# Performance work log

Hardware: AMD Instinct MI355X
Metric: run time of the kernel (lower is better)

The kernel has to match this reference:

```python
import jax, jax.numpy as jnp
import numpy as np

U, DP, TOPK, NH = 2, 16, 8, 2
D = 512
M = DP ** U          # 256 slots
DK = U * DP          # 32 addressing dim
BETA_MAX = 2.0


def setup_inputs():
    key = jax.random.key(0)
    ks = jax.random.split(key, 12)
    B, T = 8, 128
    s = 0.02
    return {
        "h": jax.random.normal(ks[0], (B, T, D), jnp.float32),
        "K_slots": jax.random.normal(ks[1], (B, M, D), jnp.float32) * s,
        "V_slots": jax.random.normal(ks[2], (B, M, D), jnp.float32) * s,
        "z_K": jnp.ones((B, M), jnp.float32),
        "z_V": jnp.ones((B, M), jnp.float32),
        "W_k": jax.random.normal(ks[3], (DK, D), jnp.float32) * s,
        "W_q": jax.random.normal(ks[4], (DK, D), jnp.float32) * s,
        "log_tau_w": jnp.zeros((1,), jnp.float32),
        "log_tau_r": jnp.zeros((1,), jnp.float32),
        "hh_k": jax.random.normal(ks[5], (NH, D, D), jnp.float32) * s,
        "hh_vk": jax.random.normal(ks[6], (NH, D, D), jnp.float32) * s,
        "hh_vv": jax.random.normal(ks[7], (NH, D, D), jnp.float32) * s,
        "hh_bw": jax.random.normal(ks[8], (NH, 1, D), jnp.float32) * s,
        "hh_bb": jnp.zeros((NH, 1), jnp.float32),
        "gamma": jnp.float32(1.0),
        "W_out": jax.random.normal(ks[9], (D, D), jnp.float32) * s,
        "W_gate": jax.random.normal(ks[10], (D, D), jnp.float32) * s,
    }


def _kron_address(z, log_tau):
    # z: [B, DK]; Kronecker-factored softmax address over M = DP**U slots
    B = z.shape[0]
    probs = jax.nn.softmax(z.reshape(B, U, DP) / jnp.exp(log_tau[0]), axis=-1)
    addr = probs[:, 0]
    for u in range(1, U):
        addr = (addr[:, :, None] * probs[:, u, None, :]).reshape(B, -1)
    w, idx = jax.lax.top_k(addr, TOPK)
    return idx, w


def _forward(h, K_slots, V_slots, z_K, z_V, W_k, W_q, log_tau_w, log_tau_r,
             hh_k, hh_vk, hh_vv, hh_bw, hh_bb, gamma, W_out, W_gate,
             checkpoint=False):
    B, T, _ = h.shape
    scale = D ** -0.5
    b_idx = jnp.arange(B)[:, None]
    sp_gamma = jax.nn.softplus(gamma)

    def step(carry, h_t):
        K_s, V_s, zK, zV = carry
        write_idx, write_w = _kron_address(h_t @ W_k.T, log_tau_w)
        read_idx, _ = _kron_address(h_t @ W_q.T, log_tau_r)
        # scatter write weights into dense [B, M] (top-k indices are unique)
        w_full = jnp.zeros((B, M), h_t.dtype).at[b_idx, write_idx].set(write_w)
        # PDMA decay
        decay = (1.0 - w_full) ** sp_gamma
        K_s = decay[..., None] * K_s
        V_s = decay[..., None] * V_s
        zK = decay * zK + w_full
        zV = decay * zV + w_full
        # gather active slots: [B, K, D]
        K_act = jnp.take_along_axis(K_s, write_idx[:, :, None], axis=1)
        V_act = jnp.take_along_axis(V_s, write_idx[:, :, None], axis=1)
        # Householder update chain
        for j in range(NH):
            k_j = jax.nn.silu(h_t @ hh_k[j].T)
            k_hat = k_j / jnp.maximum(
                jnp.linalg.norm(k_j, axis=-1, keepdims=True), 1e-12)
            v_kj = h_t @ hh_vk[j].T
            v_vj = h_t @ hh_vv[j].T
            beta = BETA_MAX * jax.nn.sigmoid(h_t @ hh_bw[j].T + hh_bb[j])  # [B,1]
            kh = k_hat[:, None, :]
            be = beta[:, None, :]
            K_act = K_act - be * kh * (kh * K_act).sum(-1, keepdims=True) \
                    + be * k_j[:, None, :] * v_kj[:, None, :]
            V_act = V_act - be * kh * (kh * V_act).sum(-1, keepdims=True) \
                    + be * k_j[:, None, :] * v_vj[:, None, :]
        # scatter updated slots back
        K_s = K_s.at[b_idx, write_idx].set(K_act)
        V_s = V_s.at[b_idx, write_idx].set(V_act)
        # read path
        K_read = jnp.take_along_axis(K_s, read_idx[:, :, None], axis=1)
        V_read = jnp.take_along_axis(V_s, read_idx[:, :, None], axis=1)
        zK_read = jnp.take_along_axis(zK, read_idx, axis=1)[..., None]
        zV_read = jnp.take_along_axis(zV, read_idx, axis=1)[..., None]
        K_n = K_read / zK_read
        V_n = V_read / zV_read
        rel = (K_n * h_t[:, None, :]).sum(-1)           # [B, K]
        attn = jax.nn.softmax(rel * scale, axis=-1)
        readout = (attn[..., None] * V_n).sum(1)        # [B, D]
        out = jax.nn.sigmoid(h_t @ W_gate.T) * (readout @ W_out.T)
        return (K_s, V_s, zK, zV), (out, write_idx, read_idx)

    step_fn = jax.checkpoint(step) if checkpoint else step
    (K_s, V_s, zK, zV), (outs, widx, ridx) = jax.lax.scan(
        step_fn, (K_slots, V_slots, z_K, z_V), jnp.swapaxes(h, 0, 1))
    return (jnp.swapaxes(outs, 0, 1), K_s, V_s, zK, zV, widx[-1], ridx[-1])


def reference(h, K_slots, V_slots, z_K, z_V, W_k, W_q, log_tau_w, log_tau_r,
              hh_k, hh_vk, hh_vv, hh_bw, hh_bb, gamma, W_out, W_gate):
    return _forward(h, K_slots, V_slots, z_K, z_V, W_k, W_q, log_tau_w,
                    log_tau_r, hh_k, hh_vk, hh_vv, hh_bw, hh_bb, gamma,
                    W_out, W_gate)
```

## Files before the change

kernel.cpp:

```cpp
#include <hip/hip_runtime.h>
#include <math.h>

#define D_ 512
#define M_ 256
#define T_ 128
#define B_ 8
#define TOPK_ 8
#define NH_ 2
#define BT_ (B_*T_)

__device__ __forceinline__ float wred(float v){
#pragma unroll
  for (int m = 1; m < 64; m <<= 1) v += __shfl_xor(v, m, 64);
  return v;
}
__device__ __forceinline__ float4 ld4(const float* p){ return *(const float4*)p; }
__device__ __forceinline__ void st4(float* p, float4 v){ *(float4*)p = v; }
__device__ __forceinline__ float dot4(float4 a, float4 b){
  return a.x*b.x + a.y*b.y + a.z*b.z + a.w*b.w;
}
__device__ __forceinline__ float4 scl4(float4 a, float s){
  a.x*=s; a.y*=s; a.z*=s; a.w*=s; return a;
}

template<int CTRL>
__device__ __forceinline__ float dpp_add(float x){
  int y = __builtin_amdgcn_update_dpp(0, __float_as_int(x), CTRL, 0xf, 0xf, true);
  return x + __int_as_float(y);
}
__device__ __forceinline__ float wredd(float x){
  x = dpp_add<0x111>(x);
  x = dpp_add<0x112>(x);
  x = dpp_add<0x114>(x);
  x = dpp_add<0x118>(x);
  x = dpp_add<0x142>(x);
  x = dpp_add<0x143>(x);
  return __int_as_float(__builtin_amdgcn_readlane(__float_as_int(x), 63));
}

__global__ __launch_bounds__(64) void addr_kernel(
    const float* __restrict__ h, const float* __restrict__ Wk,
    const float* __restrict__ Wq, const float* __restrict__ ltw,
    const float* __restrict__ ltr, const float* __restrict__ gammap,
    float* __restrict__ metab)
{
  const int bt = blockIdx.x;
  const int tid = threadIdx.x;
  __shared__ float p_s[64];

  const float* hrow = h + (size_t)bt*D_;
  const float* wrow = (tid < 32) ? (Wk + (size_t)tid*D_)
                                 : (Wq + (size_t)(tid-32)*D_);
  float dot = 0.f;
  for (int d = 0; d < D_; d += 4){
    float4 hv = ld4(&hrow[d]); float4 wv = ld4(&wrow[d]);
    dot += hv.x*wv.x + hv.y*wv.y + hv.z*wv.z + hv.w*wv.w;
  }
  float tau = (tid < 32) ? expf(ltw[0]) : expf(ltr[0]);
  float mx = dot;
#pragma unroll
  for (int m = 1; m < 16; m <<= 1) mx = fmaxf(mx, __shfl_xor(mx, m, 64));
  float e = expf((dot - mx)/tau);
  float sm = e;
#pragma unroll
  for (int m = 1; m < 16; m <<= 1) sm += __shfl_xor(sm, m, 64);
  p_s[tid] = e / sm;
  __syncthreads();

  const int half = tid >> 5;
  const int l = tid & 31;
  const int g0 = half*32, g1 = half*32 + 16;
  float av[8];
#pragma unroll
  for (int k = 0; k < 8; ++k){
    int x = l*8 + k;
    av[k] = p_s[g0 + (x>>4)] * p_s[g1 + (x&15)];
  }
  const float sp = log1pf(expf(gammap[0]));
  for (int r = 0; r < TOPK_; ++r){
    float bv = -1.f; int bi = 0;
#pragma unroll
    for (int k = 0; k < 8; ++k){ if (av[k] > bv){ bv = av[k]; bi = l*8+k; } }
#pragma unroll
    for (int m = 1; m < 32; m <<= 1){
      float ov = __shfl_xor(bv, m, 64); int oi = __shfl_xor(bi, m, 64);
      if (ov > bv || (ov == bv && oi < bi)){ bv = ov; bi = oi; }
    }
    if ((bi >> 3) == l) av[bi & 7] = -2.f;
    float* mp = metab + (size_t)(bt*TOPK_ + r)*4;
    if (tid == 0){
      mp[0] = __int_as_float(bi); mp[1] = bv; mp[2] = powf(1.f - bv, sp);
    }
    if (tid == 32) mp[3] = __int_as_float(bi);
  }
}

__global__ __launch_bounds__(256) void zscan_kernel(
    const float* __restrict__ zK0, const float* __restrict__ zV0,
    const float* __restrict__ metab, float2* __restrict__ zr,
    float* __restrict__ o_zK, float* __restrict__ o_zV)
{
  __shared__ __align__(16) float4 meta_s[T_*TOPK_];
  const int b = blockIdx.x;
  const int m = threadIdx.x;
  const float4* mb = (const float4*)metab + (size_t)b*T_*TOPK_;
#pragma unroll
  for (int q = 0; q < 4; ++q) meta_s[m + q*256] = mb[m + q*256];
  float zk = zK0[b*M_+m], zv = zV0[b*M_+m];
  __syncthreads();
  for (int t = 0; t < T_; ++t){
#pragma unroll
    for (int i = 0; i < TOPK_; ++i){
      float4 me = meta_s[t*TOPK_+i];
      if (m == __float_as_int(me.x)){ zk = me.z*zk + me.y; zv = me.z*zv + me.y; }
    }
#pragma unroll
    for (int i = 0; i < TOPK_; ++i){
      float4 me = meta_s[t*TOPK_+i];
      if (m == __float_as_int(me.w))
        zr[(size_t)(b*T_+t)*TOPK_+i] = make_float2(1.f/zk, 1.f/zv);
    }
  }
  o_zK[b*M_+m] = zk; o_zV[b*M_+m] = zv;
}

struct GemmPtrs { const float* W[6]; float* C[6]; };

__global__ __launch_bounds__(256) void gemm_nt(
    const float* __restrict__ A, GemmPtrs p)
{
  const float* W = p.W[blockIdx.z];
  float* C = p.C[blockIdx.z];
  const int n0 = blockIdx.x * 64;
  const int m0 = blockIdx.y * 64;
  const int tid = threadIdx.x;
  __shared__ __align__(16) float As[16][68];
  __shared__ __align__(16) float Bs[16][68];
  const int r  = tid >> 2;
  const int c4 = (tid & 3) << 2;
  const int tx4 = (tid & 15) << 2;
  const int ty4 = (tid >> 4) << 2;
  float acc[4][4] = {{0.f}};

  for (int kc = 0; kc < 512; kc += 16){
    float4 av = ld4(&A[(size_t)(m0+r)*512 + kc + c4]);
    float4 wv = ld4(&W[(size_t)(n0+r)*512 + kc + c4]);
    __syncthreads();
    As[c4+0][r]=av.x; As[c4+1][r]=av.y; As[c4+2][r]=av.z; As[c4+3][r]=av.w;
    Bs[c4+0][r]=wv.x; Bs[c4+1][r]=wv.y; Bs[c4+2][r]=wv.z; Bs[c4+3][r]=wv.w;
    __syncthreads();
#pragma unroll
    for (int k = 0; k < 16; ++k){
      float4 a  = ld4(&As[k][ty4]);
      float4 bq = ld4(&Bs[k][tx4]);
      acc[0][0]+=a.x*bq.x; acc[0][1]+=a.x*bq.y; acc[0][2]+=a.x*bq.z; acc[0][3]+=a.x*bq.w;
      acc[1][0]+=a.y*bq.x; acc[1][1]+=a.y*bq.y; acc[1][2]+=a.y*bq.z; acc[1][3]+=a.y*bq.w;
      acc[2][0]+=a.z*bq.x; acc[2][1]+=a.z*bq.y; acc[2][2]+=a.z*bq.z; acc[2][3]+=a.z*bq.w;
      acc[3][0]+=a.w*bq.x; acc[3][1]+=a.w*bq.y; acc[3][2]+=a.w*bq.z; acc[3][3]+=a.w*bq.w;
    }
  }
#pragma unroll
  for (int i = 0; i < 4; ++i){
    float4 cv; cv.x=acc[i][0]; cv.y=acc[i][1]; cv.z=acc[i][2]; cv.w=acc[i][3];
    st4(&C[(size_t)(m0+ty4+i)*512 + n0 + tx4], cv);
  }
}

__global__ __launch_bounds__(256) void gemm_out(
    const float* __restrict__ h, const float* __restrict__ rdo,
    const float* __restrict__ Wg, const float* __restrict__ Wo,
    float* __restrict__ C)
{
  const int n0 = blockIdx.x * 64;
  const int m0 = blockIdx.y * 64;
  const int tid = threadIdx.x;
  __shared__ __align__(16) float Ag[16][68];
  __shared__ __align__(16) float Ao[16][68];
  __shared__ __align__(16) float Bg[16][68];
  __shared__ __align__(16) float Bo[16][68];
  const int r  = tid >> 2;
  const int c4 = (tid & 3) << 2;
  const int tx4 = (tid & 15) << 2;
  const int ty4 = (tid >> 4) << 2;
  float accg[4][4] = {{0.f}};
  float acco[4][4] = {{0.f}};

  for (int kc = 0; kc < 512; kc += 16){
    float4 a1 = ld4(&h  [(size_t)(m0+r)*512 + kc + c4]);
    float4 a2 = ld4(&rdo[(size_t)(m0+r)*512 + kc + c4]);
    float4 w1 = ld4(&Wg [(size_t)(n0+r)*512 + kc + c4]);
    float4 w2 = ld4(&Wo [(size_t)(n0+r)*512 + kc + c4]);
    __syncthreads();
    Ag[c4+0][r]=a1.x; Ag[c4+1][r]=a1.y; Ag[c4+2][r]=a1.z; Ag[c4+3][r]=a1.w;
    Ao[c4+0][r]=a2.x; Ao[c4+1][r]=a2.y; Ao[c4+2][r]=a2.z; Ao[c4+3][r]=a2.w;
    Bg[c4+0][r]=w1.x; Bg[c4+1][r]=w1.y; Bg[c4+2][r]=w1.z; Bg[c4+3][r]=w1.w;
    Bo[c4+0][r]=w2.x; Bo[c4+1][r]=w2.y; Bo[c4+2][r]=w2.z; Bo[c4+3][r]=w2.w;
    __syncthreads();
#pragma unroll
    for (int k = 0; k < 16; ++k){
      float4 ag = ld4(&Ag[k][ty4]);
      float4 ao = ld4(&Ao[k][ty4]);
      float4 bg = ld4(&Bg[k][tx4]);
      float4 bo = ld4(&Bo[k][tx4]);
      accg[0][0]+=ag.x*bg.x; accg[0][1]+=ag.x*bg.y; accg[0][2]+=ag.x*bg.z; accg[0][3]+=ag.x*bg.w;
      accg[1][0]+=ag.y*bg.x; accg[1][1]+=ag.y*bg.y; accg[1][2]+=ag.y*bg.z; accg[1][3]+=ag.y*bg.w;
      accg[2][0]+=ag.z*bg.x; accg[2][1]+=ag.z*bg.y; accg[2][2]+=ag.z*bg.z; accg[2][3]+=ag.z*bg.w;
      accg[3][0]+=ag.w*bg.x; accg[3][1]+=ag.w*bg.y; accg[3][2]+=ag.w*bg.z; accg[3][3]+=ag.w*bg.w;
      acco[0][0]+=ao.x*bo.x; acco[0][1]+=ao.x*bo.y; acco[0][2]+=ao.x*bo.z; acco[0][3]+=ao.x*bo.w;
      acco[1][0]+=ao.y*bo.x; acco[1][1]+=ao.y*bo.y; acco[1][2]+=ao.y*bo.z; acco[1][3]+=ao.y*bo.w;
      acco[2][0]+=ao.z*bo.x; acco[2][1]+=ao.z*bo.y; acco[2][2]+=ao.z*bo.z; acco[2][3]+=ao.z*bo.w;
      acco[3][0]+=ao.w*bo.x; acco[3][1]+=ao.w*bo.y; acco[3][2]+=ao.w*bo.z; acco[3][3]+=ao.w*bo.w;
    }
  }
#pragma unroll
  for (int i = 0; i < 4; ++i){
    float4 cv;
    cv.x = acco[i][0] / (1.f + expf(-accg[i][0]));
    cv.y = acco[i][1] / (1.f + expf(-accg[i][1]));
    cv.z = acco[i][2] / (1.f + expf(-accg[i][2]));
    cv.w = acco[i][3] / (1.f + expf(-accg[i][3]));
    st4(&C[(size_t)(m0+ty4+i)*512 + n0 + tx4], cv);
  }
}

__global__ __launch_bounds__(256) void ew2_kernel(
    float* __restrict__ khat, float* __restrict__ kvk, float* __restrict__ kvv,
    float* __restrict__ pre2, const float* __restrict__ h,
    const float* __restrict__ hh_bw, const float* __restrict__ hh_bb)
{
  const int bt = blockIdx.x;
  const int tid = threadIdx.x;
  const int wid = tid >> 6, lane = tid & 63;
  float* k0p  = khat + (size_t)bt*D_;
  float* k1p  = khat + (size_t)BT_*D_ + (size_t)bt*D_;
  float* vk0p = kvk  + (size_t)bt*D_;
  float* vk1p = kvk  + (size_t)BT_*D_ + (size_t)bt*D_;
  float* vv0p = kvv  + (size_t)bt*D_;
  float* vv1p = kvv  + (size_t)BT_*D_ + (size_t)bt*D_;
  const float* hp  = h + (size_t)bt*D_;

  float s0[2], s1[2];
  float n0 = 0.f, n1 = 0.f, bd0 = 0.f, bd1 = 0.f;
#pragma unroll
  for (int q = 0; q < 2; ++q){
    int d = tid + q*256;
    float x0 = k0p[d], x1 = k1p[d], hv = hp[d];
    float v0 = x0 / (1.f + expf(-x0));
    float v1 = x1 / (1.f + expf(-x1));
    s0[q] = v0; s1[q] = v1;
    n0 += v0*v0; n1 += v1*v1;
    bd0 += hv*hh_bw[d]; bd1 += hv*hh_bw[D_ + d];
  }
  __shared__ float4 rb[4];
  float4 acc = make_float4(wred(n0), wred(n1), wred(bd0), wred(bd1));
  if (lane == 0) rb[wid] = acc;
  __syncthreads();
  float4 t0 = rb[0], t1 = rb[1], t2 = rb[2], t3 = rb[3];
  n0 = t0.x+t1.x+t2.x+t3.x; n1 = t0.y+t1.y+t2.y+t3.y;
  bd0 = t0.z+t1.z+t2.z+t3.z; bd1 = t0.w+t1.w+t2.w+t3.w;
  float inv0 = 1.f / fmaxf(sqrtf(n0), 1e-12f);
  float inv1 = 1.f / fmaxf(sqrtf(n1), 1e-12f);
  float be0 = 2.f / (1.f + expf(-(bd0 + hh_bb[0])));
  float be1 = 2.f / (1.f + expf(-(bd1 + hh_bb[1])));

  float c01 = 0.f, dK = 0.f, dV = 0.f;
#pragma unroll
  for (int q = 0; q < 2; ++q){
    int d = tid + q*256;
    float kh0 = s0[q]*inv0, kh1 = s1[q]*inv1;
    float u0K = s0[q]*vk0p[d], u1K = s1[q]*vk1p[d];
    float u0V = s0[q]*vv0p[d], u1V = s1[q]*vv1p[d];
    k0p[d] = kh0; k1p[d] = kh1;
    vk0p[d] = be0*u0K + be1*u1K;
    vv0p[d] = be0*u0V + be1*u1V;
    c01 += kh1*kh0; dK += kh1*u0K; dV += kh1*u0V;
  }
  __syncthreads();
  float4 acc2 = make_float4(wred(c01), wred(dK), wred(dV), 0.f);
  if (lane == 0) rb[wid] = acc2;
  __syncthreads();
  if (tid == 0){
    float4 a = rb[0], b = rb[1], c = rb[2], d = rb[3];
    pre2[(size_t)bt*8+0] = a.x+b.x+c.x+d.x;
    pre2[(size_t)bt*8+1] = a.y+b.y+c.y+d.y;
    pre2[(size_t)bt*8+2] = a.z+b.z+c.z+d.z;
    pre2[(size_t)bt*8+3] = be0;
    pre2[(size_t)bt*8+4] = be1;
  }
}

__global__ __launch_bounds__(512) void scan_kernel(
    float* __restrict__ Ks, float* __restrict__ Vs,
    const float* __restrict__ khat, const float* __restrict__ ucKb,
    const float* __restrict__ ucVb, const float* __restrict__ pre2,
    const float* __restrict__ metab, const float2* __restrict__ zr,
    const float* __restrict__ h, float* __restrict__ readout,
    float* __restrict__ o_widx, float* __restrict__ o_ridx)
{
  __shared__ __align__(16) float ring[4][4*D_];
  __shared__ __align__(16) float Vr_s[2][TOPK_][D_];
  __shared__ float2 rel2_s[2][TOPK_];

  const int b = blockIdx.x;
  const int tid = threadIdx.x;
  const int s = tid >> 6, lane = tid & 63;
  const int l4 = lane * 4;
  const float scale = 0.044194173824159216f;

  float* Ksb = Ks + (size_t)b*M_*D_;
  float* Vsb = Vs + (size_t)b*M_*D_;
  const float* vbt[4] = { khat, khat + (size_t)BT_*D_, ucKb, ucVb };
  const float* srcc = vbt[s >> 1];
  const int goff = (s & 1)*256 + l4;
  const int loff = (s >> 1)*D_ + goff;
  const float4* mb = (const float4*)metab;

  const int bt0 = b*T_;
  st4(&ring[0][loff], ld4(srcc + (size_t)bt0*D_ + goff));
  st4(&ring[1][loff], ld4(srcc + (size_t)(bt0+1)*D_ + goff));
  float4 g = ld4(srcc + (size_t)(bt0+2)*D_ + goff);

  float4 me   = mb[bt0*TOPK_ + s];
  float4 me_n = mb[(bt0+1)*TOPK_ + s];
  float4 pm   = ld4(&pre2[(size_t)bt0*8]);
  float  be1v = pre2[(size_t)bt0*8+4];
  float4 pm_n = ld4(&pre2[(size_t)(bt0+1)*8]);
  float  be1_n= pre2[(size_t)(bt0+1)*8+4];
  float2 zr2   = zr[(size_t)bt0*TOPK_ + s];
  float2 zr2_n = zr[(size_t)(bt0+1)*TOPK_ + s];

  int mi = __float_as_int(me.x);
  float4 K0 = ld4(&Ksb[(size_t)mi*D_ + l4]);
  float4 K1 = ld4(&Ksb[(size_t)mi*D_ + 256 + l4]);
  float4 V0 = ld4(&Vsb[(size_t)mi*D_ + l4]);
  float4 V1 = ld4(&Vsb[(size_t)mi*D_ + 256 + l4]);
  __syncthreads();

#pragma unroll 4
  for (int t = 0; t < T_; ++t){
    const int bt = b*T_ + t;
    const float dec = me.z;
    const int   ri  = __float_as_int(me.w);
    mi = __float_as_int(me.x);

    st4(&ring[(t+2)&3][loff], g);
    float4 HTa = ld4(h + (size_t)bt*D_ + l4);
    float4 HTb = ld4(h + (size_t)bt*D_ + 256 + l4);

    const float* rbuf = ring[t & 3];
    float4 kh0a = ld4(&rbuf[l4]),        kh0b = ld4(&rbuf[256+l4]);
    float4 kh1a = ld4(&rbuf[D_+l4]),     kh1b = ld4(&rbuf[D_+256+l4]);
    float4 ucKa = ld4(&rbuf[2*D_+l4]),   ucKb2 = ld4(&rbuf[2*D_+256+l4]);
    float4 ucVa = ld4(&rbuf[3*D_+l4]),   ucVb2 = ld4(&rbuf[3*D_+256+l4]);

    K0 = scl4(K0,dec); K1 = scl4(K1,dec);
    V0 = scl4(V0,dec); V1 = scl4(V1,dec);
    float aK = wredd(dot4(K0,kh0a) + dot4(K1,kh0b));
    float bK = wredd(dot4(K0,kh1a) + dot4(K1,kh1b));
    float aV = wredd(dot4(V0,kh0a) + dot4(V1,kh0b));
    float bV = wredd(dot4(V0,kh1a) + dot4(V1,kh1b));
    float p0K = pm.w*aK, p1K = be1v*(bK + pm.w*(pm.y - aK*pm.x));
    float p0V = pm.w*aV, p1V = be1v*(bV + pm.w*(pm.z - aV*pm.x));
    K0.x += ucKa.x  - p0K*kh0a.x - p1K*kh1a.x;
    K0.y += ucKa.y  - p0K*kh0a.y - p1K*kh1a.y;
    K0.z += ucKa.z  - p0K*kh0a.z - p1K*kh1a.z;
    K0.w += ucKa.w  - p0K*kh0a.w - p1K*kh1a.w;
    K1.x += ucKb2.x - p0K*kh0b.x - p1K*kh1b.x;
    K1.y += ucKb2.y - p0K*kh0b.y - p1K*kh1b.y;
    K1.z += ucKb2.z - p0K*kh0b.z - p1K*kh1b.z;
    K1.w += ucKb2.w - p0K*kh0b.w - p1K*kh1b.w;
    V0.x += ucVa.x  - p0V*kh0a.x - p1V*kh1a.x;
    V0.y += ucVa.y  - p0V*kh0a.y - p1V*kh1a.y;
    V0.z += ucVa.z  - p0V*kh0a.z - p1V*kh1a.z;
    V0.w += ucVa.w  - p0V*kh0a.w - p1V*kh1a.w;
    V1.x += ucVb2.x - p0V*kh0b.x - p1V*kh1b.x;
    V1.y += ucVb2.y - p0V*kh0b.y - p1V*kh1b.y;
    V1.z += ucVb2.z - p0V*kh0b.z - p1V*kh1b.z;
    V1.w += ucVb2.w - p0V*kh0b.w - p1V*kh1b.w;

    st4(&Ksb[(size_t)mi*D_ + l4], K0); st4(&Ksb[(size_t)mi*D_ + 256 + l4], K1);
    st4(&Vsb[(size_t)mi*D_ + l4], V0); st4(&Vsb[(size_t)mi*D_ + 256 + l4], V1);

    __syncthreads();

    float4 RK0 = ld4(&Ksb[(size_t)ri*D_ + l4]);
    float4 RK1 = ld4(&Ksb[(size_t)ri*D_ + 256 + l4]);
    float4 RV0 = ld4(&Vsb[(size_t)ri*D_ + l4]);
    float4 RV1 = ld4(&Vsb[(size_t)ri*D_ + 256 + l4]);
    const int mi_n = __float_as_int(me_n.x);
    float4 nK0 = ld4(&Ksb[(size_t)mi_n*D_ + l4]);
    float4 nK1 = ld4(&Ksb[(size_t)mi_n*D_ + 256 + l4]);
    float4 nV0 = ld4(&Vsb[(size_t)mi_n*D_ + l4]);
    float4 nV1 = ld4(&Vsb[(size_t)mi_n*D_ + 256 + l4]);
    const int bt3  = (t+3 < T_) ? bt+3 : b*T_+T_-1;
    const int btnn = (t+2 < T_) ? bt+2 : b*T_+T_-1;
    g = ld4(srcc + (size_t)bt3*D_ + goff);
    float4 me_nn = mb[btnn*TOPK_ + s];
    float4 pm_nn = ld4(&pre2[(size_t)btnn*8]);
    float  be1nn = pre2[(size_t)btnn*8+4];
    float2 zr2nn = zr[(size_t)btnn*TOPK_ + s];

    if (t > 0){
      const int pp = (t-1) & 1;
      float2 rz[TOPK_];
#pragma unroll
      for (int i = 0; i < TOPK_; ++i) rz[i] = rel2_s[pp][i];
      float mx = rz[0].x;
#pragma unroll
      for (int i = 1; i < TOPK_; ++i) mx = fmaxf(mx, rz[i].x);
      float smm = 0.f, r = 0.f;
#pragma unroll
      for (int i = 0; i < TOPK_; ++i){
        float ev = __expf(rz[i].x - mx); smm += ev;
        r += ev * rz[i].y * Vr_s[pp][i][tid];
      }
      readout[(size_t)(bt-1)*D_ + tid] = r * __builtin_amdgcn_rcpf(smm);
    }

    float dt = wredd(dot4(RK0,HTa) + dot4(RK1,HTb));
    if (lane == 0)
      rel2_s[t&1][s] = make_float2(dt * scale * zr2.x, zr2.y);
    st4(&Vr_s[t&1][s][l4], RV0); st4(&Vr_s[t&1][s][256+l4], RV1);

    K0=nK0; K1=nK1; V0=nV0; V1=nV1;
    me=me_n; pm=pm_n; be1v=be1_n; zr2=zr2_n;
    me_n=me_nn; pm_n=pm_nn; be1_n=be1nn; zr2_n=zr2nn;
  }

  __syncthreads();
  {
    const int btL = b*T_ + T_ - 1;
    const int pp = (T_-1) & 1;
    float2 rz[TOPK_];
#pragma unroll
    for (int i = 0; i < TOPK_; ++i) rz[i] = rel2_s[pp][i];
    float mx = rz[0].x;
#pragma unroll
    for (int i = 1; i < TOPK_; ++i) mx = fmaxf(mx, rz[i].x);
    float smm = 0.f, r = 0.f;
#pragma unroll
    for (int i = 0; i < TOPK_; ++i){
      float ev = __expf(rz[i].x - mx); smm += ev;
      r += ev * rz[i].y * Vr_s[pp][i][tid];
    }
    readout[(size_t)btL*D_ + tid] = r * __builtin_amdgcn_rcpf(smm);

    if (tid < TOPK_){
      float4 m = mb[btL*TOPK_ + tid];
      o_widx[b*TOPK_+tid] = (float)__float_as_int(m.x);
      o_ridx[b*TOPK_+tid] = (float)__float_as_int(m.w);
    }
  }
}

extern "C" void kernel_launch(void* const* d_in, const int* in_sizes, int n_in,
                              void* d_out, int out_size, void* d_ws, size_t ws_size,
                              hipStream_t stream)
{
  (void)in_sizes; (void)n_in; (void)out_size; (void)ws_size;
  const float* h       = (const float*)d_in[0];
  const float* K_slots = (const float*)d_in[1];
  const float* V_slots = (const float*)d_in[2];
  const float* z_K     = (const float*)d_in[3];
  const float* z_V     = (const float*)d_in[4];
  const float* W_k     = (const float*)d_in[5];
  const float* W_q     = (const float*)d_in[6];
  const float* ltw     = (const float*)d_in[7];
  const float* ltr     = (const float*)d_in[8];
  const float* hh_k    = (const float*)d_in[9];
  const float* hh_vk   = (const float*)d_in[10];
  const float* hh_vv   = (const float*)d_in[11];
  const float* hh_bw   = (const float*)d_in[12];
  const float* hh_bb   = (const float*)d_in[13];
  const float* gamma   = (const float*)d_in[14];
  const float* W_out   = (const float*)d_in[15];
  const float* W_gate  = (const float*)d_in[16];

  float* out    = (float*)d_out;
  float* o_outs = out;
  float* o_Ks   = out + 524288;
  float* o_Vs   = out + 1572864;
  float* o_zK   = out + 2621440;
  float* o_zV   = out + 2623488;
  float* o_widx = out + 2625536;
  float* o_ridx = out + 2625600;

  float* ws    = (float*)d_ws;
  float* khat  = ws;
  float* kvk   = ws + 2*(size_t)BT_*D_;
  float* kvv   = kvk + 2*(size_t)BT_*D_;
  float* rdo   = kvv + 2*(size_t)BT_*D_;
  float* metab = rdo + (size_t)BT_*D_;
  float* pre2  = metab + (size_t)BT_*TOPK_*4;
  float2* zrb  = (float2*)(pre2 + (size_t)BT_*8);

  (void)hipMemcpyAsync(o_Ks, K_slots, sizeof(float)*(size_t)B_*M_*D_,
                       hipMemcpyDeviceToDevice, stream);
  (void)hipMemcpyAsync(o_Vs, V_slots, sizeof(float)*(size_t)B_*M_*D_,
                       hipMemcpyDeviceToDevice, stream);

  addr_kernel<<<BT_, 64, 0, stream>>>(h, W_k, W_q, ltw, ltr, gamma, metab);
  zscan_kernel<<<B_, 256, 0, stream>>>(z_K, z_V, metab, zrb, o_zK, o_zV);

  GemmPtrs p{};
  p.W[0] = hh_k;           p.C[0] = khat;
  p.W[1] = hh_k + 262144;  p.C[1] = khat + (size_t)BT_*D_;
  p.W[2] = hh_vk;          p.C[2] = kvk;
  p.W[3] = hh_vk + 262144; p.C[3] = kvk + (size_t)BT_*D_;
  p.W[4] = hh_vv;          p.C[4] = kvv;
  p.W[5] = hh_vv + 262144; p.C[5] = kvv + (size_t)BT_*D_;
  gemm_nt<<<dim3(8,16,6), 256, 0, stream>>>(h, p);

  ew2_kernel<<<BT_, 256, 0, stream>>>(khat, kvk, kvv, pre2, h, hh_bw, hh_bb);

  scan_kernel<<<B_, 512, 0, stream>>>(o_Ks, o_Vs, khat, kvk, kvv,
                                      pre2, metab, zrb, h, rdo,
                                      o_widx, o_ridx);

  gemm_out<<<dim3(8,16), 256, 0, stream>>>(h, rdo, W_gate, W_out, o_outs);
}
```

Baseline: 541.6 us.

## Prefetch scan operands to registers, double-buffer gemm_nt, drop zscan LDS staging

In scan_kernel, the shared-memory ring that staged khat/ucK/ucV rows is replaced by loading each warp's full rows directly from global memory into registers one step ahead. This removes the LDS ring writes and reads but duplicates global/L2 traffic across the eight warps. gemm_nt now double-buffers its LDS tiles, so the next tile's global loads overlap compute and the loop needs one barrier per k-step instead of two. zscan drops its shared-memory metadata preload and reads metadata from global memory each step.

```diff
diff --git a/kernel.cpp b/kernel.cpp
--- a/kernel.cpp
+++ b/kernel.cpp
@@ -100,24 +100,23 @@
     const float* __restrict__ metab, float2* __restrict__ zr,
     float* __restrict__ o_zK, float* __restrict__ o_zV)
 {
-  __shared__ __align__(16) float4 meta_s[T_*TOPK_];
   const int b = blockIdx.x;
   const int m = threadIdx.x;
   const float4* mb = (const float4*)metab + (size_t)b*T_*TOPK_;
-#pragma unroll
-  for (int q = 0; q < 4; ++q) meta_s[m + q*256] = mb[m + q*256];
   float zk = zK0[b*M_+m], zv = zV0[b*M_+m];
-  __syncthreads();
   for (int t = 0; t < T_; ++t){
+    float4 me[TOPK_];
+#pragma unroll
+    for (int i = 0; i < TOPK_; ++i) me[i] = mb[t*TOPK_+i];
 #pragma unroll
     for (int i = 0; i < TOPK_; ++i){
-      float4 me = meta_s[t*TOPK_+i];
-      if (m == __float_as_int(me.x)){ zk = me.z*zk + me.y; zv = me.z*zv + me.y; }
+      if (m == __float_as_int(me[i].x)){
+        zk = me[i].z*zk + me[i].y; zv = me[i].z*zv + me[i].y;
+      }
     }
 #pragma unroll
     for (int i = 0; i < TOPK_; ++i){
-      float4 me = meta_s[t*TOPK_+i];
-      if (m == __float_as_int(me.w))
+      if (m == __float_as_int(me[i].w))
         zr[(size_t)(b*T_+t)*TOPK_+i] = make_float2(1.f/zk, 1.f/zv);
     }
   }
@@ -134,29 +133,43 @@
   const int n0 = blockIdx.x * 64;
   const int m0 = blockIdx.y * 64;
   const int tid = threadIdx.x;
-  __shared__ __align__(16) float As[16][68];
-  __shared__ __align__(16) float Bs[16][68];
+  __shared__ __align__(16) float As[2][16][68];
+  __shared__ __align__(16) float Bs[2][16][68];
   const int r  = tid >> 2;
   const int c4 = (tid & 3) << 2;
   const int tx4 = (tid & 15) << 2;
   const int ty4 = (tid >> 4) << 2;
   float acc[4][4] = {{0.f}};
 
-  for (int kc = 0; kc < 512; kc += 16){
-    float4 av = ld4(&A[(size_t)(m0+r)*512 + kc + c4]);
-    float4 wv = ld4(&W[(size_t)(n0+r)*512 + kc + c4]);
-    __syncthreads();
-    As[c4+0][r]=av.x; As[c4+1][r]=av.y; As[c4+2][r]=av.z; As[c4+3][r]=av.w;
-    Bs[c4+0][r]=wv.x; Bs[c4+1][r]=wv.y; Bs[c4+2][r]=wv.z; Bs[c4+3][r]=wv.w;
-    __syncthreads();
+  {
+    float4 av = ld4(&A[(size_t)(m0+r)*512 + c4]);
+    float4 wv = ld4(&W[(size_t)(n0+r)*512 + c4]);
+    As[0][c4+0][r]=av.x; As[0][c4+1][r]=av.y; As[0][c4+2][r]=av.z; As[0][c4+3][r]=av.w;
+    Bs[0][c4+0][r]=wv.x; Bs[0][c4+1][r]=wv.y; Bs[0][c4+2][r]=wv.z; Bs[0][c4+3][r]=wv.w;
+  }
+  __syncthreads();
+
+  for (int kc = 0, buf = 0; kc < 512; kc += 16, buf ^= 1){
+    float4 av, wv;
+    const bool more = (kc + 16 < 512);
+    if (more){
+      av = ld4(&A[(size_t)(m0+r)*512 + kc + 16 + c4]);
+      wv = ld4(&W[(size_t)(n0+r)*512 + kc + 16 + c4]);
+    }
 #pragma unroll
     for (int k = 0; k < 16; ++k){
-      float4 a  = ld4(&As[k][ty4]);
-      float4 bq = ld4(&Bs[k][tx4]);
+      float4 a  = ld4(&As[buf][k][ty4]);
+      float4 bq = ld4(&Bs[buf][k][tx4]);
       acc[0][0]+=a.x*bq.x; acc[0][1]+=a.x*bq.y; acc[0][2]+=a.x*bq.z; acc[0][3]+=a.x*bq.w;
       acc[1][0]+=a.y*bq.x; acc[1][1]+=a.y*bq.y; acc[1][2]+=a.y*bq.z; acc[1][3]+=a.y*bq.w;
       acc[2][0]+=a.z*bq.x; acc[2][1]+=a.z*bq.y; acc[2][2]+=a.z*bq.z; acc[2][3]+=a.z*bq.w;
       acc[3][0]+=a.w*bq.x; acc[3][1]+=a.w*bq.y; acc[3][2]+=a.w*bq.z; acc[3][3]+=a.w*bq.w;
+    }
+    if (more){
+      int nb = buf ^ 1;
+      As[nb][c4+0][r]=av.x; As[nb][c4+1][r]=av.y; As[nb][c4+2][r]=av.z; As[nb][c4+3][r]=av.w;
+      Bs[nb][c4+0][r]=wv.x; Bs[nb][c4+1][r]=wv.y; Bs[nb][c4+2][r]=wv.z; Bs[nb][c4+3][r]=wv.w;
+      __syncthreads();
     }
   }
 #pragma unroll
@@ -291,13 +304,12 @@
 
 __global__ __launch_bounds__(512) void scan_kernel(
     float* __restrict__ Ks, float* __restrict__ Vs,
-    const float* __restrict__ khat, const float* __restrict__ ucKb,
-    const float* __restrict__ ucVb, const float* __restrict__ pre2,
+    const float* __restrict__ khat, const float* __restrict__ ucKp,
+    const float* __restrict__ ucVp, const float* __restrict__ pre2,
     const float* __restrict__ metab, const float2* __restrict__ zr,
     const float* __restrict__ h, float* __restrict__ readout,
     float* __restrict__ o_widx, float* __restrict__ o_ridx)
 {
-  __shared__ __align__(16) float ring[4][4*D_];
   __shared__ __align__(16) float Vr_s[2][TOPK_][D_];
   __shared__ float2 rel2_s[2][TOPK_];
 
@@ -309,16 +321,16 @@
 
   float* Ksb = Ks + (size_t)b*M_*D_;
   float* Vsb = Vs + (size_t)b*M_*D_;
-  const float* vbt[4] = { khat, khat + (size_t)BT_*D_, ucKb, ucVb };
-  const float* srcc = vbt[s >> 1];
-  const int goff = (s & 1)*256 + l4;
-  const int loff = (s >> 1)*D_ + goff;
+  const float* kh0p = khat;
+  const float* kh1p = khat + (size_t)BT_*D_;
   const float4* mb = (const float4*)metab;
 
   const int bt0 = b*T_;
-  st4(&ring[0][loff], ld4(srcc + (size_t)bt0*D_ + goff));
-  st4(&ring[1][loff], ld4(srcc + (size_t)(bt0+1)*D_ + goff));
-  float4 g = ld4(srcc + (size_t)(bt0+2)*D_ + goff);
+  size_t o0 = (size_t)bt0*D_ + l4;
+  float4 c_kh0a = ld4(kh0p+o0), c_kh0b = ld4(kh0p+o0+256);
+  float4 c_kh1a = ld4(kh1p+o0), c_kh1b = ld4(kh1p+o0+256);
+  float4 c_uKa  = ld4(ucKp+o0), c_uKb  = ld4(ucKp+o0+256);
+  float4 c_uVa  = ld4(ucVp+o0), c_uVb  = ld4(ucVp+o0+256);
 
   float4 me   = mb[bt0*TOPK_ + s];
   float4 me_n = mb[(bt0+1)*TOPK_ + s];
@@ -334,49 +346,47 @@
   float4 K1 = ld4(&Ksb[(size_t)mi*D_ + 256 + l4]);
   float4 V0 = ld4(&Vsb[(size_t)mi*D_ + l4]);
   float4 V1 = ld4(&Vsb[(size_t)mi*D_ + 256 + l4]);
-  __syncthreads();
-
-#pragma unroll 4
+
+#pragma unroll 2
   for (int t = 0; t < T_; ++t){
     const int bt = b*T_ + t;
     const float dec = me.z;
     const int   ri  = __float_as_int(me.w);
     mi = __float_as_int(me.x);
 
-    st4(&ring[(t+2)&3][loff], g);
+    const int btn = (t+1 < T_) ? bt+1 : bt;
+    size_t on = (size_t)btn*D_ + l4;
+    float4 n_kh0a = ld4(kh0p+on), n_kh0b = ld4(kh0p+on+256);
+    float4 n_kh1a = ld4(kh1p+on), n_kh1b = ld4(kh1p+on+256);
+    float4 n_uKa  = ld4(ucKp+on), n_uKb  = ld4(ucKp+on+256);
+    float4 n_uVa  = ld4(ucVp+on), n_uVb  = ld4(ucVp+on+256);
     float4 HTa = ld4(h + (size_t)bt*D_ + l4);
     float4 HTb = ld4(h + (size_t)bt*D_ + 256 + l4);
 
-    const float* rbuf = ring[t & 3];
-    float4 kh0a = ld4(&rbuf[l4]),        kh0b = ld4(&rbuf[256+l4]);
-    float4 kh1a = ld4(&rbuf[D_+l4]),     kh1b = ld4(&rbuf[D_+256+l4]);
-    float4 ucKa = ld4(&rbuf[2*D_+l4]),   ucKb2 = ld4(&rbuf[2*D_+256+l4]);
-    float4 ucVa = ld4(&rbuf[3*D_+l4]),   ucVb2 = ld4(&rbuf[3*D_+256+l4]);
-
     K0 = scl4(K0,dec); K1 = scl4(K1,dec);
     V0 = scl4(V0,dec); V1 = scl4(V1,dec);
-    float aK = wredd(dot4(K0,kh0a) + dot4(K1,kh0b));
-    float bK = wredd(dot4(K0,kh1a) + dot4(K1,kh1b));
-    float aV = wredd(dot4(V0,kh0a) + dot4(V1,kh0b));
-    float bV = wredd(dot4(V0,kh1a) + dot4(V1,kh1b));
+    float aK = wredd(dot4(K0,c_kh0a) + dot4(K1,c_kh0b));
+    float bK = wredd(dot4(K0,c_kh1a) + dot4(K1,c_kh1b));
+    float aV = wredd(dot4(V0,c_kh0a) + dot4(V1,c_kh0b));
+    float bV = wredd(dot4(V0,c_kh1a) + dot4(V1,c_kh1b));
     float p0K = pm.w*aK, p1K = be1v*(bK + pm.w*(pm.y - aK*pm.x));
     float p0V = pm.w*aV, p1V = be1v*(bV + pm.w*(pm.z - aV*pm.x));
-    K0.x += ucKa.x  - p0K*kh0a.x - p1K*kh1a.x;
-    K0.y += ucKa.y  - p0K*kh0a.y - p1K*kh1a.y;
-    K0.z += ucKa.z  - p0K*kh0a.z - p1K*kh1a.z;
-    K0.w += ucKa.w  - p0K*kh0a.w - p1K*kh1a.w;
-    K1.x += ucKb2.x - p0K*kh0b.x - p1K*kh1b.x;
-    K1.y += ucKb2.y - p0K*kh0b.y - p1K*kh1b.y;
-    K1.z += ucKb2.z - p0K*kh0b.z - p1K*kh1b.z;
-    K1.w += ucKb2.w - p0K*kh0b.w - p1K*kh1b.w;
-    V0.x += ucVa.x  - p0V*kh0a.x - p1V*kh1a.x;
-    V0.y += ucVa.y  - p0V*kh0a.y - p1V*kh1a.y;
-    V0.z += ucVa.z  - p0V*kh0a.z - p1V*kh1a.z;
-    V0.w += ucVa.w  - p0V*kh0a.w - p1V*kh1a.w;
-    V1.x += ucVb2.x - p0V*kh0b.x - p1V*kh1b.x;
-    V1.y += ucVb2.y - p0V*kh0b.y - p1V*kh1b.y;
-    V1.z += ucVb2.z - p0V*kh0b.z - p1V*kh1b.z;
-    V1.w += ucVb2.w - p0V*kh0b.w - p1V*kh1b.w;
+    K0.x += c_uKa.x - p0K*c_kh0a.x - p1K*c_kh1a.x;
+    K0.y += c_uKa.y - p0K*c_kh0a.y - p1K*c_kh1a.y;
+    K0.z += c_uKa.z - p0K*c_kh0a.z - p1K*c_kh1a.z;
+    K0.w += c_uKa.w - p0K*c_kh0a.w - p1K*c_kh1a.w;
+    K1.x += c_uKb.x - p0K*c_kh0b.x - p1K*c_kh1b.x;
+    K1.y += c_uKb.y - p0K*c_kh0b.y - p1K*c_kh1b.y;
+    K1.z += c_uKb.z - p0K*c_kh0b.z - p1K*c_kh1b.z;
+    K1.w += c_uKb.w - p0K*c_kh0b.w - p1K*c_kh1b.w;
+    V0.x += c_uVa.x - p0V*c_kh0a.x - p1V*c_kh1a.x;
+    V0.y += c_uVa.y - p0V*c_kh0a.y - p1V*c_kh1a.y;
+    V0.z += c_uVa.z - p0V*c_kh0a.z - p1V*c_kh1a.z;
+    V0.w += c_uVa.w - p0V*c_kh0a.w - p1V*c_kh1a.w;
+    V1.x += c_uVb.x - p0V*c_kh0b.x - p1V*c_kh1b.x;
+    V1.y += c_uVb.y - p0V*c_kh0b.y - p1V*c_kh1b.y;
+    V1.z += c_uVb.z - p0V*c_kh0b.z - p1V*c_kh1b.z;
+    V1.w += c_uVb.w - p0V*c_kh0b.w - p1V*c_kh1b.w;
 
     st4(&Ksb[(size_t)mi*D_ + l4], K0); st4(&Ksb[(size_t)mi*D_ + 256 + l4], K1);
     st4(&Vsb[(size_t)mi*D_ + l4], V0); st4(&Vsb[(size_t)mi*D_ + 256 + l4], V1);
@@ -392,9 +402,7 @@
     float4 nK1 = ld4(&Ksb[(size_t)mi_n*D_ + 256 + l4]);
     float4 nV0 = ld4(&Vsb[(size_t)mi_n*D_ + l4]);
     float4 nV1 = ld4(&Vsb[(size_t)mi_n*D_ + 256 + l4]);
-    const int bt3  = (t+3 < T_) ? bt+3 : b*T_+T_-1;
     const int btnn = (t+2 < T_) ? bt+2 : b*T_+T_-1;
-    g = ld4(srcc + (size_t)bt3*D_ + goff);
     float4 me_nn = mb[btnn*TOPK_ + s];
     float4 pm_nn = ld4(&pre2[(size_t)btnn*8]);
     float  be1nn = pre2[(size_t)btnn*8+4];
@@ -425,6 +433,8 @@
     K0=nK0; K1=nK1; V0=nV0; V1=nV1;
     me=me_n; pm=pm_n; be1v=be1_n; zr2=zr2_n;
     me_n=me_nn; pm_n=pm_nn; be1_n=be1nn; zr2_n=zr2nn;
+    c_kh0a=n_kh0a; c_kh0b=n_kh0b; c_kh1a=n_kh1a; c_kh1b=n_kh1b;
+    c_uKa=n_uKa; c_uKb=n_uKb; c_uVa=n_uVa; c_uVb=n_uVb;
   }
 
   __syncthreads();
```

Result: no change. 533.7 us (-1.5%).
